# Kernel optimization log

Measured on AMD Instinct MI355X. Metric: run time of the kernel, lower is better.

The kernel has to match this reference:

```python
import jax, jax.numpy as jnp
import numpy as np

B, INS, OUTS, REF, H, NH, DH, NL, DFF = 8, 32, 64, 8, 256, 8, 32, 6, 1024
N = OUTS * OUTS  # 4096 tokens


def _ln(x, g, b, eps=1e-5):
    m = x.mean(-1, keepdims=True)
    v = ((x - m) ** 2).mean(-1, keepdims=True)
    return (x - m) * jax.lax.rsqrt(v + eps) * g + b


def _resize_ac(x, out):
    Hin = x.shape[1]
    c = jnp.arange(out) * ((Hin - 1) / (out - 1))
    i0 = jnp.floor(c).astype(jnp.int32)
    i1 = jnp.minimum(i0 + 1, Hin - 1)
    w = (c - i0).astype(x.dtype)
    x = x[:, i0] * (1 - w)[None, :, None, None] + x[:, i1] * w[None, :, None, None]
    x = x[:, :, i0] * (1 - w)[None, None, :, None] + x[:, :, i1] * w[None, None, :, None]
    return x


def _pos_embedding():
    # unified_pos_embedding: distance from each 64x64 grid point to each 8x8 ref point -> [N, REF^2]
    g = jnp.linspace(0.0, 1.0, OUTS)
    gx, gy = jnp.meshgrid(g, g, indexing='ij')
    grid = jnp.stack([gx, gy], -1).reshape(N, 2)
    r = jnp.linspace(0.0, 1.0, REF)
    rx, ry = jnp.meshgrid(r, r, indexing='ij')
    rgrid = jnp.stack([rx, ry], -1).reshape(REF * REF, 2)
    return jnp.sqrt(((grid[:, None, :] - rgrid[None, :, :]) ** 2).sum(-1))


def setup_inputs() -> dict:
    key = jax.random.key(0)
    ks = iter(jax.random.split(key, 64))
    def nrm(shape, std=0.02):
        return jax.random.normal(next(ks), shape, jnp.float32) * std
    inp = {'x': jax.random.normal(next(ks), (B, INS, INS, 3), jnp.float32)}
    inp['pre_W1'] = nrm((1 + REF * REF, 2 * H)); inp['pre_b1'] = jnp.zeros((2 * H,))
    inp['pre_W2'] = nrm((2 * H, H)); inp['pre_b2'] = jnp.zeros((H,))
    inp['placeholder'] = jax.random.uniform(next(ks), (H,), jnp.float32) / H
    inp['ln1_g'] = jnp.ones((NL, H)); inp['ln1_b'] = jnp.zeros((NL, H))
    inp['ln1a_g'] = jnp.ones((NL, H)); inp['ln1a_b'] = jnp.zeros((NL, H))
    inp['Wq'] = nrm((NL, H, H)); inp['Wk'] = nrm((NL, H, H)); inp['Wv'] = nrm((NL, H, H))
    inp['Wo'] = nrm((NL, H, H)); inp['bo'] = jnp.zeros((NL, H))
    inp['kn_g'] = jnp.ones((NL, NH, DH)); inp['kn_b'] = jnp.zeros((NL, NH, DH))
    inp['vn_g'] = jnp.ones((NL, NH, DH)); inp['vn_b'] = jnp.zeros((NL, NH, DH))
    inp['ln2_g'] = jnp.ones((NL, H)); inp['ln2_b'] = jnp.zeros((NL, H))
    inp['mlp_W1'] = nrm((NL, H, DFF)); inp['mlp_b1'] = jnp.zeros((NL, DFF))
    inp['mlp_W2'] = nrm((NL, DFF, H)); inp['mlp_b2'] = jnp.zeros((NL, H))
    inp['ln3_g'] = jnp.ones((H,)); inp['ln3_b'] = jnp.zeros((H,))
    inp['out_W'] = nrm((H, 1)); inp['out_b'] = jnp.zeros((1,))
    return inp


def reference(x, pre_W1, pre_b1, pre_W2, pre_b2, placeholder,
              ln1_g, ln1_b, ln1a_g, ln1a_b, Wq, Wk, Wv, Wo, bo,
              kn_g, kn_b, vn_g, vn_b, ln2_g, ln2_b,
              mlp_W1, mlp_b1, mlp_W2, mlp_b2, ln3_g, ln3_b, out_W, out_b):
    Bsz = x.shape[0]
    xr = _resize_ac(x, OUTS)[..., 2:3]          # [B,64,64,1]
    fx = xr.reshape(Bsz, N, 1)
    pos = _pos_embedding()                       # [N,64]
    fx = jnp.concatenate([fx, jnp.broadcast_to(pos[None], (Bsz, N, REF * REF))], -1)
    h = jax.nn.gelu(fx @ pre_W1 + pre_b1, approximate=False) @ pre_W2 + pre_b2
    h = h + placeholder
    for i in range(NL):
        xq = _ln(h, ln1_g[i], ln1_b[i])
        xkv = _ln(h, ln1a_g[i], ln1a_b[i])
        q = (xq @ Wq[i]).reshape(Bsz, N, NH, DH).transpose(0, 2, 1, 3)
        k = (xkv @ Wk[i]).reshape(Bsz, N, NH, DH).transpose(0, 2, 1, 3)
        v = (xkv @ Wv[i]).reshape(Bsz, N, NH, DH).transpose(0, 2, 1, 3)
        # galerkin attention: layernorm K and V over head dim (per-head affine), no softmax
        k = _ln(k, kn_g[i][:, None, :], kn_b[i][:, None, :])
        v = _ln(v, vn_g[i][:, None, :], vn_b[i][:, None, :])
        ctx = jnp.einsum('bhnd,bhne->bhde', k, v) / N   # [B,h,d,d]
        att = jnp.einsum('bhnd,bhde->bhne', q, ctx)
        att = att.transpose(0, 2, 1, 3).reshape(Bsz, N, H) @ Wo[i] + bo[i]
        h = h + att
        y = _ln(h, ln2_g[i], ln2_b[i])
        h = h + (jax.nn.gelu(y @ mlp_W1[i] + mlp_b1[i], approximate=False) @ mlp_W2[i] + mlp_b2[i])
    out = _ln(h, ln3_g, ln3_b) @ out_W + out_b
    return out.reshape(Bsz, OUTS, OUTS, 1)
```

## Files before the change

### kernel.cpp

```cpp
#include <hip/hip_runtime.h>
#include <cmath>

#define B_    8
#define INS_  32
#define OUTS_ 64
#define REF_  8
#define H_    256
#define NH_   8
#define DH_   32
#define NL_   6
#define DFF_  1024
#define N_    4096
#define M_    (B_*N_)
#define BUF   8388608ull

typedef unsigned short u16;
typedef unsigned int   u32;
typedef __attribute__((ext_vector_type(8))) short  bf16x8;
typedef __attribute__((ext_vector_type(4))) float  f32x4;
typedef __attribute__((ext_vector_type(4))) unsigned short u16x4;

struct bfpair { u16 hi, lo; };

__device__ __forceinline__ float gelu_f(float x){
    return 0.5f * x * (1.0f + erff(x * 0.70710678118654752f));
}
__device__ __forceinline__ u16 f2b(float f){
    union { float f; u32 u; } v; v.f = f;
    u32 r = v.u + 0x7fffu + ((v.u >> 16) & 1u);
    return (u16)(r >> 16);
}
__device__ __forceinline__ float b2f(u16 b){
    union { u32 u; float f; } v; v.u = ((u32)b) << 16;
    return v.f;
}
__device__ __forceinline__ bfpair fsplit(float x){
    bfpair p;
    p.hi = f2b(x);
    p.lo = f2b(x - b2f(p.hi));
    return p;
}

__global__ __launch_bounds__(256) void tconv_kernel(const float* __restrict__ in,
                                                    u16* __restrict__ oh,
                                                    u16* __restrict__ ol,
                                                    int K, int N, int Kpad, int nl,
                                                    int lstride)
{
    int idx = blockIdx.x * 256 + threadIdx.x;
    int per = N * Kpad;
    if (idx >= nl * per) return;
    int l = idx / per;
    int rem = idx - l * per;
    int n = rem / Kpad;
    int k = rem - n * Kpad;
    float v = (k < K) ? in[(size_t)l * K * N + (size_t)k * N + n] : 0.0f;
    bfpair p = fsplit(v);
    size_t o = (size_t)l * lstride + (size_t)n * Kpad + k;
    oh[o] = p.hi; ol[o] = p.lo;
}

__global__ __launch_bounds__(256) void lnfold_kernel(const float* __restrict__ kg,
                                                     const float* __restrict__ kb,
                                                     const float* __restrict__ vg,
                                                     const float* __restrict__ vb,
                                                     float* __restrict__ lng,
                                                     float* __restrict__ lnb)
{
    int idx = blockIdx.x * 256 + threadIdx.x;
    if (idx >= NL_ * 512) return;
    int l = idx >> 9, c = idx & 511;
    if (c < 256) { lng[idx] = kg[l * 256 + c];       lnb[idx] = kb[l * 256 + c]; }
    else         { lng[idx] = vg[l * 256 + c - 256]; lnb[idx] = vb[l * 256 + c - 256]; }
}

__global__ __launch_bounds__(256) void fx_kernel(const float* __restrict__ x,
                                                 u16* __restrict__ fh,
                                                 u16* __restrict__ fl)
{
    int idx = blockIdx.x * 256 + threadIdx.x;
    const int total = M_ * 96;
    if (idx >= total) return;
    int f   = idx % 96;
    int row = idx / 96;
    int n   = row % N_;
    int b   = row / N_;
    int gi = n >> 6, gj = n & 63;
    float v = 0.0f;
    if (f == 0) {
        float ci = gi * (31.0f / 63.0f);
        float cj = gj * (31.0f / 63.0f);
        int i0 = (int)floorf(ci); int i1 = min(i0 + 1, 31);
        int j0 = (int)floorf(cj); int j1 = min(j0 + 1, 31);
        float wi = ci - (float)i0, wj = cj - (float)j0;
        const float* xb = x + (size_t)b * INS_ * INS_ * 3 + 2;
        float v00 = xb[(i0 * 32 + j0) * 3];
        float v01 = xb[(i0 * 32 + j1) * 3];
        float v10 = xb[(i1 * 32 + j0) * 3];
        float v11 = xb[(i1 * 32 + j1) * 3];
        float r0 = v00 * (1.0f - wi) + v10 * wi;
        float r1 = v01 * (1.0f - wi) + v11 * wi;
        v = r0 * (1.0f - wj) + r1 * wj;
    } else if (f < 65) {
        int r = f - 1;
        int ri = r >> 3, rj = r & 7;
        float dx = gi * (1.0f / 63.0f) - ri * (1.0f / 7.0f);
        float dy = gj * (1.0f / 63.0f) - rj * (1.0f / 7.0f);
        v = sqrtf(dx * dx + dy * dy);
    }
    bfpair p = fsplit(v);
    fh[idx] = p.hi; fl[idx] = p.lo;
}

template<int EPI, int BN, int TERMS>
__global__ __launch_bounds__(256) void gemm_split(const u16* __restrict__ Ah,
                                                  const u16* __restrict__ Al,
                                                  const u16* __restrict__ Bh,
                                                  const u16* __restrict__ Bl,
                                                  float* __restrict__ Cf,
                                                  u16* __restrict__ Ch,
                                                  u16* __restrict__ Cl,
                                                  const float* __restrict__ bias,
                                                  const float* __restrict__ bias2,
                                                  const float* __restrict__ lng,
                                                  const float* __restrict__ lnb,
                                                  int M, int Nn, int K, int bstride)
{
    constexpr int NREP = BN / 32;
    constexpr int BROUNDS = BN / 64;
    __shared__ u16 AsH[2][4096];
    __shared__ u16 BsH[2][BN * 32];
    __shared__ u16 AsL[TERMS >= 2 ? 2 : 1][TERMS >= 2 ? 4096 : 1];
    __shared__ u16 BsL[TERMS == 3 ? 2 : 1][TERMS == 3 ? BN * 32 : 1];
    const int tid = threadIdx.x;
    const int nwgx = gridDim.x;
    const int nwg  = nwgx * gridDim.y;
    const int bid  = blockIdx.y * nwgx + blockIdx.x;
    const int swz  = (bid & 7) * (nwg >> 3) + (bid >> 3);
    const int bm = (swz / nwgx) * 128;
    const int bn = (swz % nwgx) * BN;
    const u16* BhB = Bh + (size_t)(bm >> 12) * bstride;
    const u16* BlB = Bl + (size_t)(bm >> 12) * bstride;
    const int l  = tid & 63;
    const int w  = tid >> 6;
    const int wr = w >> 1, wc = w & 1;
    const int lrow = l & 15;
    const int kh   = l >> 4;

    auto stage = [&](int k0, int s) {
        #pragma unroll
        for (int i = 0; i < 2; ++i) {
            int L = i * 256 + tid;
            int row = L >> 2, ch = L & 3;
            size_t goffA = (size_t)(bm + row) * K + k0 + ch * 8;
            __builtin_amdgcn_global_load_lds(
                (const __attribute__((address_space(1))) void*)(Ah + goffA),
                (__attribute__((address_space(3))) void*)(&AsH[s][L * 8]), 16, 0, 0);
            if constexpr (TERMS >= 2)
                __builtin_amdgcn_global_load_lds(
                    (const __attribute__((address_space(1))) void*)(Al + goffA),
                    (__attribute__((address_space(3))) void*)(&AsL[s][L * 8]), 16, 0, 0);
        }
        #pragma unroll
        for (int i = 0; i < BROUNDS; ++i) {
            int L = i * 256 + tid;
            int row = L >> 2, ch = L & 3;
            size_t goffB = (size_t)(bn + row) * K + k0 + ch * 8;
            __builtin_amdgcn_global_load_lds(
                (const __attribute__((address_space(1))) void*)(BhB + goffB),
                (__attribute__((address_space(3))) void*)(&BsH[s][L * 8]), 16, 0, 0);
            if constexpr (TERMS == 3)
                __builtin_amdgcn_global_load_lds(
                    (const __attribute__((address_space(1))) void*)(BlB + goffB),
                    (__attribute__((address_space(3))) void*)(&BsL[s][L * 8]), 16, 0, 0);
        }
    };

    f32x4 acc[4][NREP];
    #pragma unroll
    for (int m = 0; m < 4; ++m)
        #pragma unroll
        for (int n = 0; n < NREP; ++n)
            acc[m][n] = (f32x4){0.0f, 0.0f, 0.0f, 0.0f};

    const int nk = K >> 5;
    stage(0, 0);
    __syncthreads();
    int cur = 0;
    for (int t = 0; t < nk; ++t) {
        if (t + 1 < nk) stage((t + 1) << 5, cur ^ 1);
        bf16x8 afh[4], afl[4], bfh[NREP], bfl[NREP];
        #pragma unroll
        for (int m = 0; m < 4; ++m) {
            int off = (wr * 64 + m * 16 + lrow) * 32 + kh * 8;
            afh[m] = *(const bf16x8*)(&AsH[cur][off]);
            if constexpr (TERMS >= 2) afl[m] = *(const bf16x8*)(&AsL[cur][off]);
        }
        #pragma unroll
        for (int n = 0; n < NREP; ++n) {
            int off = (wc * (BN / 2) + n * 16 + lrow) * 32 + kh * 8;
            bfh[n] = *(const bf16x8*)(&BsH[cur][off]);
            if constexpr (TERMS == 3) bfl[n] = *(const bf16x8*)(&BsL[cur][off]);
        }
        #pragma unroll
        for (int m = 0; m < 4; ++m)
            #pragma unroll
            for (int n = 0; n < NREP; ++n) {
                acc[m][n] = __builtin_amdgcn_mfma_f32_16x16x32_bf16(afh[m], bfh[n], acc[m][n], 0, 0, 0);
                if constexpr (TERMS >= 2)
                    acc[m][n] = __builtin_amdgcn_mfma_f32_16x16x32_bf16(afl[m], bfh[n], acc[m][n], 0, 0, 0);
                if constexpr (TERMS == 3)
                    acc[m][n] = __builtin_amdgcn_mfma_f32_16x16x32_bf16(afh[m], bfl[n], acc[m][n], 0, 0, 0);
            }
        __syncthreads();
        cur ^= 1;
    }

    const int row0 = bm + wr * 64;
    const int col0 = bn + wc * (BN / 2);

    if constexpr (EPI == 4) {
        #pragma unroll
        for (int m = 0; m < 4; ++m) {
            #pragma unroll
            for (int j = 0; j < 4; ++j) {
                int r = row0 + m * 16 + kh * 4 + j;
                #pragma unroll
                for (int hp = 0; hp < NREP / 2; ++hp) {
                    float a0 = acc[m][2 * hp + 0][j];
                    float a1 = acc[m][2 * hp + 1][j];
                    float s = a0 + a1;
                    s += __shfl_xor(s, 1); s += __shfl_xor(s, 2);
                    s += __shfl_xor(s, 4); s += __shfl_xor(s, 8);
                    float mean = s * (1.0f / 32.0f);
                    float d0 = a0 - mean, d1 = a1 - mean;
                    float q = d0 * d0 + d1 * d1;
                    q += __shfl_xor(q, 1); q += __shfl_xor(q, 2);
                    q += __shfl_xor(q, 4); q += __shfl_xor(q, 8);
                    float rstd = rsqrtf(q * (1.0f / 32.0f) + 1e-5f);
                    #pragma unroll
                    for (int t = 0; t < 2; ++t) {
                        int n = 2 * hp + t;
                        int col = col0 + n * 16 + lrow;
                        float dd = t ? d1 : d0;
                        float o = dd * rstd * lng[col] + lnb[col];
                        bfpair p = fsplit(o);
                        size_t idx = (size_t)r * Nn + col;
                        Ch[idx] = p.hi; Cl[idx] = p.lo;
                    }
                }
            }
        }
        return;
    }

    #pragma unroll
    for (int m = 0; m < 4; ++m) {
        #pragma unroll
        for (int n = 0; n < NREP; ++n) {
            int col = col0 + n * 16 + lrow;
            float bv = bias ? bias[col] : 0.0f;
            if (EPI == 3) bv += bias2[col];
            #pragma unroll
            for (int j = 0; j < 4; ++j) {
                int r = row0 + m * 16 + kh * 4 + j;
                float v = acc[m][n][j] + bv;
                size_t idx = (size_t)r * Nn + col;
                if (EPI == 0) {
                    bfpair p = fsplit(v);
                    Ch[idx] = p.hi; Cl[idx] = p.lo;
                } else if (EPI == 1) {
                    bfpair p = fsplit(gelu_f(v));
                    Ch[idx] = p.hi; Cl[idx] = p.lo;
                } else if (EPI == 2) {
                    Cf[idx] += v;
                } else {
                    Cf[idx] = v;
                }
            }
        }
    }
}

__global__ __launch_bounds__(256) void ln_dual_kernel(const float* __restrict__ h,
                                                      u16* __restrict__ o1h,
                                                      u16* __restrict__ o1l,
                                                      u16* __restrict__ o2h,
                                                      u16* __restrict__ o2l,
                                                      const float* __restrict__ g1,
                                                      const float* __restrict__ b1,
                                                      const float* __restrict__ g2,
                                                      const float* __restrict__ b2)
{
    int row  = blockIdx.x * 4 + (threadIdx.x >> 6);
    int lane = threadIdx.x & 63;
    const float4 v = ((const float4*)(h + (size_t)row * H_))[lane];
    float s = v.x + v.y + v.z + v.w;
    #pragma unroll
    for (int m = 1; m < 64; m <<= 1) s += __shfl_xor(s, m, 64);
    float mean = s * (1.0f / H_);
    float dx = v.x - mean, dy = v.y - mean, dz = v.z - mean, dw = v.w - mean;
    float sq = dx * dx + dy * dy + dz * dz + dw * dw;
    #pragma unroll
    for (int m = 1; m < 64; m <<= 1) sq += __shfl_xor(sq, m, 64);
    float rstd = rsqrtf(sq * (1.0f / H_) + 1e-5f);

    float4 G = ((const float4*)g1)[lane];
    float4 Bv = ((const float4*)b1)[lane];
    u16x4 oh, ol;
    bfpair p0 = fsplit(dx * rstd * G.x + Bv.x);
    bfpair p1 = fsplit(dy * rstd * G.y + Bv.y);
    bfpair p2 = fsplit(dz * rstd * G.z + Bv.z);
    bfpair p3 = fsplit(dw * rstd * G.w + Bv.w);
    oh.x = p0.hi; ol.x = p0.lo;
    oh.y = p1.hi; ol.y = p1.lo;
    oh.z = p2.hi; ol.z = p2.lo;
    oh.w = p3.hi; ol.w = p3.lo;
    ((u16x4*)(o1h + (size_t)row * H_))[lane] = oh;
    ((u16x4*)(o1l + (size_t)row * H_))[lane] = ol;
    if (o2h) {
        G = ((const float4*)g2)[lane];
        Bv = ((const float4*)b2)[lane];
        p0 = fsplit(dx * rstd * G.x + Bv.x);
        p1 = fsplit(dy * rstd * G.y + Bv.y);
        p2 = fsplit(dz * rstd * G.z + Bv.z);
        p3 = fsplit(dw * rstd * G.w + Bv.w);
        oh.x = p0.hi; ol.x = p0.lo;
        oh.y = p1.hi; ol.y = p1.lo;
        oh.z = p2.hi; ol.z = p2.lo;
        oh.w = p3.hi; ol.w = p3.lo;
        ((u16x4*)(o2h + (size_t)row * H_))[lane] = oh;
        ((u16x4*)(o2l + (size_t)row * H_))[lane] = ol;
    }
}

__global__ __launch_bounds__(256) void ctx_partial_kernel(const u16* __restrict__ kvh,
                                                          const u16* __restrict__ kvl,
                                                          float* __restrict__ ctxp)
{
    int bh = blockIdx.x;
    int split = blockIdx.y;
    int b = bh >> 3, hd = bh & 7;
    __shared__ float kc[64][32], vc[64][32];
    int tid = threadIdx.x;
    int d  = tid >> 3;
    int e0 = (tid & 7) * 4;
    float a0 = 0, a1 = 0, a2 = 0, a3 = 0;
    int nbase = split * 512;
    for (int it = 0; it < 8; ++it) {
        #pragma unroll
        for (int i = 0; i < 8; ++i) {
            int elem = i * 256 + tid;
            int row = elem >> 5, col = elem & 31;
            size_t off = ((size_t)(b * N_ + nbase + it * 64 + row)) * 512 + hd * 32 + col;
            kc[row][col] = b2f(kvh[off]) + b2f(kvl[off]);
            vc[row][col] = b2f(kvh[off + 256]) + b2f(kvl[off + 256]);
        }
        __syncthreads();
        #pragma unroll
        for (int r = 0; r < 64; ++r) {
            float kd = kc[r][d];
            a0 += kd * vc[r][e0 + 0];
            a1 += kd * vc[r][e0 + 1];
            a2 += kd * vc[r][e0 + 2];
            a3 += kd * vc[r][e0 + 3];
        }
        __syncthreads();
    }
    float* out = ctxp + ((size_t)(split * 64 + bh)) * 1024 + d * 32 + e0;
    out[0] = a0; out[1] = a1; out[2] = a2; out[3] = a3;
}

__global__ __launch_bounds__(256) void compose1_kernel(const float* __restrict__ ctxp,
                                                       const float* __restrict__ Wo,
                                                       float* __restrict__ G)
{
    int b  = blockIdx.x >> 3;
    int hd = blockIdx.x & 7;
    __shared__ float cl[32][32];
    __shared__ float wl[32][256];
    int tid = threadIdx.x;
    {
        const float* src = ctxp + ((size_t)(b * 8 + hd)) * 1024;
        #pragma unroll
        for (int i = 0; i < 4; ++i) {
            float s = 0.0f;
            #pragma unroll
            for (int sp = 0; sp < 8; ++sp)
                s += src[(size_t)sp * 65536 + tid + 256 * i];
            ((float*)cl)[tid + 256 * i] = s * (1.0f / N_);
        }
        #pragma unroll
        for (int i = 0; i < 32; ++i)
            wl[i][tid] = Wo[(size_t)(hd * 32 + i) * 256 + tid];
    }
    __syncthreads();
    int j = tid;
    for (int d = 0; d < 32; ++d) {
        float s = 0.0f;
        #pragma unroll
        for (int e = 0; e < 32; ++e) s += cl[d][e] * wl[e][j];
        G[((size_t)b * 256 + hd * 32 + d) * 256 + j] = s;
    }
}

__global__ __launch_bounds__(256) void compose2_kernel(const float* __restrict__ Wq,
                                                       const float* __restrict__ G,
                                                       u16* __restrict__ fh,
                                                       u16* __restrict__ fl)
{
    int b  = blockIdx.x;
    int jg = blockIdx.y;
    __shared__ float Gs[16][256];
    int tid = threadIdx.x;
    #pragma unroll
    for (int jj = 0; jj < 16; ++jj)
        Gs[jj][tid] = G[(size_t)b * 65536 + (size_t)tid * 256 + jg * 16 + jj];
    __syncthreads();
    int i = tid;
    float acc[16];
    #pragma unroll
    for (int jj = 0; jj < 16; ++jj) acc[jj] = 0.0f;
    for (int m = 0; m < 256; ++m) {
        float wv = Wq[(size_t)i * 256 + m];
        #pragma unroll
        for (int jj = 0; jj < 16; ++jj) acc[jj] += wv * Gs[jj][m];
    }
    #pragma unroll
    for (int jj = 0; jj < 16; ++jj) {
        bfpair p = fsplit(acc[jj]);
        size_t off = (size_t)b * 65536 + (size_t)(jg * 16 + jj) * 256 + i;
        fh[off] = p.hi; fl[off] = p.lo;
    }
}

__global__ __launch_bounds__(256) void final_kernel(const float* __restrict__ h,
                                                    const float* __restrict__ g,
                                                    const float* __restrict__ bb,
                                                    const float* __restrict__ W,
                                                    const float* __restrict__ ob,
                                                    float* __restrict__ out)
{
    int row  = blockIdx.x * 4 + (threadIdx.x >> 6);
    int lane = threadIdx.x & 63;
    const float4 v = ((const float4*)(h + (size_t)row * H_))[lane];
    float s = v.x + v.y + v.z + v.w;
    #pragma unroll
    for (int m = 1; m < 64; m <<= 1) s += __shfl_xor(s, m, 64);
    float mean = s * (1.0f / H_);
    float dx = v.x - mean, dy = v.y - mean, dz = v.z - mean, dw = v.w - mean;
    float sq = dx * dx + dy * dy + dz * dz + dw * dw;
    #pragma unroll
    for (int m = 1; m < 64; m <<= 1) sq += __shfl_xor(sq, m, 64);
    float rstd = rsqrtf(sq * (1.0f / H_) + 1e-5f);
    float4 G = ((const float4*)g)[lane];
    float4 Bv = ((const float4*)bb)[lane];
    float4 Wv = ((const float4*)W)[lane];
    float s2 = (dx * rstd * G.x + Bv.x) * Wv.x
             + (dy * rstd * G.y + Bv.y) * Wv.y
             + (dz * rstd * G.z + Bv.z) * Wv.z
             + (dw * rstd * G.w + Bv.w) * Wv.w;
    #pragma unroll
    for (int m = 1; m < 64; m <<= 1) s2 += __shfl_xor(s2, m, 64);
    if (lane == 0) out[row] = s2 + ob[0];
}

extern "C" void kernel_launch(void* const* d_in, const int* in_sizes, int n_in,
                              void* d_out, int out_size, void* d_ws, size_t ws_size,
                              hipStream_t stream)
{
    const float* x        = (const float*)d_in[0];
    const float* pre_W1   = (const float*)d_in[1];
    const float* pre_b1   = (const float*)d_in[2];
    const float* pre_W2   = (const float*)d_in[3];
    const float* pre_b2   = (const float*)d_in[4];
    const float* placeholder = (const float*)d_in[5];
    const float* ln1_g    = (const float*)d_in[6];
    const float* ln1_b    = (const float*)d_in[7];
    const float* ln1a_g   = (const float*)d_in[8];
    const float* ln1a_b   = (const float*)d_in[9];
    const float* Wq       = (const float*)d_in[10];
    const float* Wk       = (const float*)d_in[11];
    const float* Wv       = (const float*)d_in[12];
    const float* Wo       = (const float*)d_in[13];
    const float* bo       = (const float*)d_in[14];
    const float* kn_g     = (const float*)d_in[15];
    const float* kn_b     = (const float*)d_in[16];
    const float* vn_g     = (const float*)d_in[17];
    const float* vn_b     = (const float*)d_in[18];
    const float* ln2_g    = (const float*)d_in[19];
    const float* ln2_b    = (const float*)d_in[20];
    const float* mlp_W1   = (const float*)d_in[21];
    const float* mlp_b1   = (const float*)d_in[22];
    const float* mlp_W2   = (const float*)d_in[23];
    const float* mlp_b2   = (const float*)d_in[24];
    const float* ln3_g    = (const float*)d_in[25];
    const float* ln3_b    = (const float*)d_in[26];
    const float* out_W    = (const float*)d_in[27];
    const float* out_b    = (const float*)d_in[28];

    float* ws   = (float*)d_ws;
    float* h    = ws;
    float* ctxp = ws + BUF;
    float* Gbuf = ctxp + 524288;
    float* lng  = Gbuf + 524288;
    float* lnb  = lng + NL_ * 512;
    u16* ub = (u16*)(lnb + NL_ * 512);
    u16* xa_h = ub;
    u16* xa_l = xa_h + BUF;
    u16* xb_h = xa_l + BUF;
    u16* xb_l = xb_h + BUF;
    u16* kv_h = xb_l + BUF;
    u16* kv_l = kv_h + 2 * BUF;
    u16* wt   = kv_l + 2 * BUF;
    u16* w_pre1h = wt;               u16* w_pre1l = w_pre1h + 49152;
    u16* w_pre2h = w_pre1l + 49152;  u16* w_pre2l = w_pre2h + 131072;
    u16* w_kvh = w_pre2l + 131072;   u16* w_kvl = w_kvh + 786432;
    u16* w_m1h = w_kvl + 786432;     u16* w_m1l = w_m1h + 1572864;
    u16* w_m2h = w_m1l + 1572864;    u16* w_m2l = w_m2h + 1572864;
    u16* f_h   = w_m2l + 1572864;    u16* f_l   = f_h + 524288;

    tconv_kernel<<<(512 * 96 + 255) / 256, 256, 0, stream>>>(pre_W1, w_pre1h, w_pre1l, 65, 512, 96, 1, 49152);
    tconv_kernel<<<(256 * 512 + 255) / 256, 256, 0, stream>>>(pre_W2, w_pre2h, w_pre2l, 512, 256, 512, 1, 131072);
    tconv_kernel<<<(6 * 65536 + 255) / 256, 256, 0, stream>>>(Wk, w_kvh, w_kvl, 256, 256, 256, 6, 131072);
    tconv_kernel<<<(6 * 65536 + 255) / 256, 256, 0, stream>>>(Wv, w_kvh + 65536, w_kvl + 65536, 256, 256, 256, 6, 131072);
    tconv_kernel<<<(6 * 262144 + 255) / 256, 256, 0, stream>>>(mlp_W1, w_m1h, w_m1l, 256, 1024, 256, 6, 262144);
    tconv_kernel<<<(6 * 262144 + 255) / 256, 256, 0, stream>>>(mlp_W2, w_m2h, w_m2l, 1024, 256, 1024, 6, 262144);
    lnfold_kernel<<<(NL_ * 512 + 255) / 256, 256, 0, stream>>>(kn_g, kn_b, vn_g, vn_b, lng, lnb);

    fx_kernel<<<(M_ * 96 + 255) / 256, 256, 0, stream>>>(x, xa_h, xa_l);
    gemm_split<1, 128, 3><<<dim3(512 / 128, M_ / 128), 256, 0, stream>>>(
        xa_h, xa_l, w_pre1h, w_pre1l, nullptr, kv_h, kv_l,
        pre_b1, nullptr, nullptr, nullptr, M_, 512, 96, 0);
    gemm_split<3, 128, 3><<<dim3(256 / 128, M_ / 128), 256, 0, stream>>>(
        kv_h, kv_l, w_pre2h, w_pre2l, h, nullptr, nullptr,
        pre_b2, placeholder, nullptr, nullptr, M_, 256, 512, 0);

    for (int l = 0; l < NL_; ++l) {
        ln_dual_kernel<<<M_ / 4, 256, 0, stream>>>(
            h, xa_h, xa_l, xb_h, xb_l, ln1_g + l * H_, ln1_b + l * H_,
            ln1a_g + l * H_, ln1a_b + l * H_);

        gemm_split<4, 128, 2><<<dim3(512 / 128, M_ / 128), 256, 0, stream>>>(
            xb_h, xb_l, w_kvh + (size_t)l * 131072, w_kvl + (size_t)l * 131072,
            nullptr, kv_h, kv_l, nullptr, nullptr,
            lng + l * 512, lnb + l * 512, M_, 512, H_, 0);

        ctx_partial_kernel<<<dim3(64, 8), 256, 0, stream>>>(kv_h, kv_l, ctxp);
        compose1_kernel<<<64, 256, 0, stream>>>(ctxp, Wo + (size_t)l * 65536, Gbuf);
        compose2_kernel<<<dim3(8, 16), 256, 0, stream>>>(Wq + (size_t)l * 65536, Gbuf, f_h, f_l);

        gemm_split<2, 64, 2><<<dim3(256 / 64, M_ / 128), 256, 0, stream>>>(
            xa_h, xa_l, f_h, f_l, h, nullptr, nullptr, bo + l * H_, nullptr,
            nullptr, nullptr, M_, H_, H_, 65536);

        ln_dual_kernel<<<M_ / 4, 256, 0, stream>>>(
            h, xa_h, xa_l, nullptr, nullptr, ln2_g + l * H_, ln2_b + l * H_, nullptr, nullptr);

        for (int half = 0; half < 2; ++half) {
            size_t ao = (size_t)half * (M_ / 2) * H_;
            gemm_split<1, 128, 3><<<dim3(DFF_ / 128, (M_ / 2) / 128), 256, 0, stream>>>(
                xa_h + ao, xa_l + ao, w_m1h + (size_t)l * 262144, w_m1l + (size_t)l * 262144,
                nullptr, xb_h, kv_h, mlp_b1 + (size_t)l * DFF_, nullptr,
                nullptr, nullptr, M_ / 2, DFF_, H_, 0);
            gemm_split<2, 64, 3><<<dim3(256 / 64, (M_ / 2) / 128), 256, 0, stream>>>(
                xb_h, kv_h, w_m2h + (size_t)l * 262144, w_m2l + (size_t)l * 262144,
                h + ao, nullptr, nullptr, mlp_b2 + (size_t)l * H_, nullptr,
                nullptr, nullptr, M_ / 2, H_, DFF_, 0);
        }
    }

    final_kernel<<<M_ / 4, 256, 0, stream>>>(
        h, ln3_g, ln3_b, out_W, out_b, (float*)d_out);
}
```

Before: 2.067 ms.

## Use single-buffered 64-wide K tiles in split-bf16 GEMM, pad first-layer K to 128

The GEMM main loop switches from a double-buffered 32-wide K slice to a single-buffered 64-wide K slice. Each slice is loaded and synchronised, then consumed as two MFMA sub-steps, which halves the number of barriers and loop trips. The loads for the next slice no longer overlap with compute, so the kernel relies on occupancy to hide memory latency. Because K must now be a multiple of 64, the first pre-layer input features and weights are padded from 96 to 128, which adds some wasted work in that GEMM.

After: 2.043 ms. Within noise of the previous version (-1.2%).

```diff
diff --git a/kernel.cpp b/kernel.cpp
--- a/kernel.cpp
+++ b/kernel.cpp
@@ -79,10 +79,10 @@
                                                  u16* __restrict__ fl)
 {
     int idx = blockIdx.x * 256 + threadIdx.x;
-    const int total = M_ * 96;
+    const int total = M_ * 128;
     if (idx >= total) return;
-    int f   = idx % 96;
-    int row = idx / 96;
+    int f   = idx & 127;
+    int row = idx >> 7;
     int n   = row % N_;
     int b   = row / N_;
     int gi = n >> 6, gj = n & 63;
@@ -127,11 +127,10 @@
                                                   int M, int Nn, int K, int bstride)
 {
     constexpr int NREP = BN / 32;
-    constexpr int BROUNDS = BN / 64;
-    __shared__ u16 AsH[2][4096];
-    __shared__ u16 BsH[2][BN * 32];
-    __shared__ u16 AsL[TERMS >= 2 ? 2 : 1][TERMS >= 2 ? 4096 : 1];
-    __shared__ u16 BsL[TERMS == 3 ? 2 : 1][TERMS == 3 ? BN * 32 : 1];
+    __shared__ u16 AsH[128 * 64];
+    __shared__ u16 BsH[BN * 64];
+    __shared__ u16 AsL[TERMS >= 2 ? 128 * 64 : 1];
+    __shared__ u16 BsL[TERMS == 3 ? BN * 64 : 1];
     const int tid = threadIdx.x;
     const int nwgx = gridDim.x;
     const int nwg  = nwgx * gridDim.y;
@@ -147,32 +146,32 @@
     const int lrow = l & 15;
     const int kh   = l >> 4;
 
-    auto stage = [&](int k0, int s) {
-        #pragma unroll
-        for (int i = 0; i < 2; ++i) {
+    auto stage = [&](int k0) {
+        #pragma unroll
+        for (int i = 0; i < 4; ++i) {
             int L = i * 256 + tid;
-            int row = L >> 2, ch = L & 3;
+            int row = L >> 3, ch = L & 7;
             size_t goffA = (size_t)(bm + row) * K + k0 + ch * 8;
             __builtin_amdgcn_global_load_lds(
                 (const __attribute__((address_space(1))) void*)(Ah + goffA),
-                (__attribute__((address_space(3))) void*)(&AsH[s][L * 8]), 16, 0, 0);
+                (__attribute__((address_space(3))) void*)(AsH + L * 8), 16, 0, 0);
             if constexpr (TERMS >= 2)
                 __builtin_amdgcn_global_load_lds(
                     (const __attribute__((address_space(1))) void*)(Al + goffA),
-                    (__attribute__((address_space(3))) void*)(&AsL[s][L * 8]), 16, 0, 0);
-        }
-        #pragma unroll
-        for (int i = 0; i < BROUNDS; ++i) {
+                    (__attribute__((address_space(3))) void*)(AsL + L * 8), 16, 0, 0);
+        }
+        #pragma unroll
+        for (int i = 0; i < BN / 32; ++i) {
             int L = i * 256 + tid;
-            int row = L >> 2, ch = L & 3;
+            int row = L >> 3, ch = L & 7;
             size_t goffB = (size_t)(bn + row) * K + k0 + ch * 8;
             __builtin_amdgcn_global_load_lds(
                 (const __attribute__((address_space(1))) void*)(BhB + goffB),
-                (__attribute__((address_space(3))) void*)(&BsH[s][L * 8]), 16, 0, 0);
+                (__attribute__((address_space(3))) void*)(BsH + L * 8), 16, 0, 0);
             if constexpr (TERMS == 3)
                 __builtin_amdgcn_global_load_lds(
                     (const __attribute__((address_space(1))) void*)(BlB + goffB),
-                    (__attribute__((address_space(3))) void*)(&BsL[s][L * 8]), 16, 0, 0);
+                    (__attribute__((address_space(3))) void*)(BsL + L * 8), 16, 0, 0);
         }
     };
 
@@ -183,37 +182,37 @@
         for (int n = 0; n < NREP; ++n)
             acc[m][n] = (f32x4){0.0f, 0.0f, 0.0f, 0.0f};
 
-    const int nk = K >> 5;
-    stage(0, 0);
-    __syncthreads();
-    int cur = 0;
+    const int nk = K >> 6;
     for (int t = 0; t < nk; ++t) {
-        if (t + 1 < nk) stage((t + 1) << 5, cur ^ 1);
-        bf16x8 afh[4], afl[4], bfh[NREP], bfl[NREP];
-        #pragma unroll
-        for (int m = 0; m < 4; ++m) {
-            int off = (wr * 64 + m * 16 + lrow) * 32 + kh * 8;
-            afh[m] = *(const bf16x8*)(&AsH[cur][off]);
-            if constexpr (TERMS >= 2) afl[m] = *(const bf16x8*)(&AsL[cur][off]);
-        }
-        #pragma unroll
-        for (int n = 0; n < NREP; ++n) {
-            int off = (wc * (BN / 2) + n * 16 + lrow) * 32 + kh * 8;
-            bfh[n] = *(const bf16x8*)(&BsH[cur][off]);
-            if constexpr (TERMS == 3) bfl[n] = *(const bf16x8*)(&BsL[cur][off]);
-        }
-        #pragma unroll
-        for (int m = 0; m < 4; ++m)
+        stage(t << 6);
+        __syncthreads();
+        #pragma unroll
+        for (int kk = 0; kk < 2; ++kk) {
+            bf16x8 afh[4], afl[4], bfh[NREP], bfl[NREP];
+            #pragma unroll
+            for (int m = 0; m < 4; ++m) {
+                int off = (wr * 64 + m * 16 + lrow) * 64 + kk * 32 + kh * 8;
+                afh[m] = *(const bf16x8*)(AsH + off);
+                if constexpr (TERMS >= 2) afl[m] = *(const bf16x8*)(AsL + off);
+            }
             #pragma unroll
             for (int n = 0; n < NREP; ++n) {
-                acc[m][n] = __builtin_amdgcn_mfma_f32_16x16x32_bf16(afh[m], bfh[n], acc[m][n], 0, 0, 0);
-                if constexpr (TERMS >= 2)
-                    acc[m][n] = __builtin_amdgcn_mfma_f32_16x16x32_bf16(afl[m], bfh[n], acc[m][n], 0, 0, 0);
-                if constexpr (TERMS == 3)
-                    acc[m][n] = __builtin_amdgcn_mfma_f32_16x16x32_bf16(afh[m], bfl[n], acc[m][n], 0, 0, 0);
+                int off = (wc * (BN / 2) + n * 16 + lrow) * 64 + kk * 32 + kh * 8;
+                bfh[n] = *(const bf16x8*)(BsH + off);
+                if constexpr (TERMS == 3) bfl[n] = *(const bf16x8*)(BsL + off);
             }
-        __syncthreads();
-        cur ^= 1;
+            #pragma unroll
+            for (int m = 0; m < 4; ++m)
+                #pragma unroll
+                for (int n = 0; n < NREP; ++n) {
+                    acc[m][n] = __builtin_amdgcn_mfma_f32_16x16x32_bf16(afh[m], bfh[n], acc[m][n], 0, 0, 0);
+                    if constexpr (TERMS >= 2)
+                        acc[m][n] = __builtin_amdgcn_mfma_f32_16x16x32_bf16(afl[m], bfh[n], acc[m][n], 0, 0, 0);
+                    if constexpr (TERMS == 3)
+                        acc[m][n] = __builtin_amdgcn_mfma_f32_16x16x32_bf16(afh[m], bfl[n], acc[m][n], 0, 0, 0);
+                }
+        }
+        if (t + 1 < nk) __syncthreads();
     }
 
     const int row0 = bm + wr * 64;
@@ -513,14 +512,14 @@
     u16* kv_h = xb_l + BUF;
     u16* kv_l = kv_h + 2 * BUF;
     u16* wt   = kv_l + 2 * BUF;
-    u16* w_pre1h = wt;               u16* w_pre1l = w_pre1h + 49152;
-    u16* w_pre2h = w_pre1l + 49152;  u16* w_pre2l = w_pre2h + 131072;
+    u16* w_pre1h = wt;               u16* w_pre1l = w_pre1h + 65536;
+    u16* w_pre2h = w_pre1l + 65536;  u16* w_pre2l = w_pre2h + 131072;
     u16* w_kvh = w_pre2l + 131072;   u16* w_kvl = w_kvh + 786432;
     u16* w_m1h = w_kvl + 786432;     u16* w_m1l = w_m1h + 1572864;
     u16* w_m2h = w_m1l + 1572864;    u16* w_m2l = w_m2h + 1572864;
     u16* f_h   = w_m2l + 1572864;    u16* f_l   = f_h + 524288;
 
-    tconv_kernel<<<(512 * 96 + 255) / 256, 256, 0, stream>>>(pre_W1, w_pre1h, w_pre1l, 65, 512, 96, 1, 49152);
+    tconv_kernel<<<(512 * 128 + 255) / 256, 256, 0, stream>>>(pre_W1, w_pre1h, w_pre1l, 65, 512, 128, 1, 65536);
     tconv_kernel<<<(256 * 512 + 255) / 256, 256, 0, stream>>>(pre_W2, w_pre2h, w_pre2l, 512, 256, 512, 1, 131072);
     tconv_kernel<<<(6 * 65536 + 255) / 256, 256, 0, stream>>>(Wk, w_kvh, w_kvl, 256, 256, 256, 6, 131072);
     tconv_kernel<<<(6 * 65536 + 255) / 256, 256, 0, stream>>>(Wv, w_kvh + 65536, w_kvl + 65536, 256, 256, 256, 6, 131072);
@@ -528,10 +527,10 @@
     tconv_kernel<<<(6 * 262144 + 255) / 256, 256, 0, stream>>>(mlp_W2, w_m2h, w_m2l, 1024, 256, 1024, 6, 262144);
     lnfold_kernel<<<(NL_ * 512 + 255) / 256, 256, 0, stream>>>(kn_g, kn_b, vn_g, vn_b, lng, lnb);
 
-    fx_kernel<<<(M_ * 96 + 255) / 256, 256, 0, stream>>>(x, xa_h, xa_l);
+    fx_kernel<<<(M_ * 128 + 255) / 256, 256, 0, stream>>>(x, xa_h, xa_l);
     gemm_split<1, 128, 3><<<dim3(512 / 128, M_ / 128), 256, 0, stream>>>(
         xa_h, xa_l, w_pre1h, w_pre1l, nullptr, kv_h, kv_l,
-        pre_b1, nullptr, nullptr, nullptr, M_, 512, 96, 0);
+        pre_b1, nullptr, nullptr, nullptr, M_, 512, 128, 0);
     gemm_split<3, 128, 3><<<dim3(256 / 128, M_ / 128), 256, 0, stream>>>(
         kv_h, kv_l, w_pre2h, w_pre2l, h, nullptr, nullptr,
         pre_b2, placeholder, nullptr, nullptr, M_, 256, 512, 0);
```
